# Optimization experiments

Measured on AMD Instinct MI355X. Metric: run time of the kernel, lower is better.

## Reference

```python
import jax, jax.numpy as jnp
import numpy as np

B_SZ, L_SEQ, D_MODEL, D_STATE = 4, 2048, 1024, 16


def setup_inputs() -> dict:
    key = jax.random.key(0)
    ks = jax.random.split(key, 6)
    x = jax.random.normal(ks[0], (B_SZ, L_SEQ, D_MODEL), jnp.float32)
    # HiPPO-inspired init: A_log = log(arange(1..n)).clamp(min=-7), broadcast over channels
    A_log = jnp.clip(jnp.log(jnp.arange(1, D_STATE + 1, dtype=jnp.float32)), -7.0, None)
    A_log = jnp.broadcast_to(A_log[None, :], (D_MODEL, D_STATE)).astype(jnp.float32)
    B_param = 0.02 * jax.random.normal(ks[1], (D_MODEL, D_STATE), jnp.float32)
    C_param = 0.02 * jax.random.normal(ks[2], (D_MODEL, D_STATE), jnp.float32)
    log_dt = 0.01 * jax.random.normal(ks[3], (D_MODEL,), jnp.float32) - 4.0
    in_w = jax.random.normal(ks[4], (2 * D_MODEL, D_MODEL), jnp.float32) / np.sqrt(D_MODEL).astype(np.float32)
    in_b = jnp.zeros((2 * D_MODEL,), jnp.float32)
    out_w = jax.random.normal(ks[5], (D_MODEL, D_MODEL), jnp.float32) / np.sqrt(D_MODEL).astype(np.float32)
    out_b = jnp.zeros((D_MODEL,), jnp.float32)
    ln_g = jnp.ones((D_MODEL,), jnp.float32)
    ln_b = jnp.zeros((D_MODEL,), jnp.float32)
    return {"x": x, "A_log": A_log, "B_param": B_param, "C_param": C_param,
            "log_dt": log_dt, "in_w": in_w, "in_b": in_b, "out_w": out_w,
            "out_b": out_b, "ln_g": ln_g, "ln_b": ln_b}


def _ssm_scan(u, A_log, B_param, C_param, log_dt):
    # u: (B, L, D). Builds kernel h[t,d] = sum_n A_bar[d,n]^t * C[d,n]*B[d,n]*dt[d]
    # and applies a causal depthwise convolution (via FFT; same math as conv1d).
    L = u.shape[1]
    dt = jnp.clip(jnp.exp(log_dt), 1e-4, 1.0)                      # (D,)
    A_bar = jnp.exp(-jnp.exp(A_log) * dt[:, None])                 # ZOH discretisation (D,N)
    A_bar = jnp.clip(A_bar, 1e-8, 1.0 - 1e-8)
    log_A = jnp.log(A_bar)                                         # (D,N)
    t_idx = jnp.arange(L, dtype=jnp.float32)                       # (L,)
    A_powers = jnp.exp(t_idx[:, None, None] * log_A[None, :, :])   # (L,D,N)
    cb_dt = C_param * B_param * dt[:, None]                        # (D,N)
    kernel = jnp.einsum('ldn,dn->ld', A_powers, cb_dt)             # (L,D)
    # causal conv: y[b,t,d] = sum_{tau<=t} kernel[tau,d] * u[b,t-tau,d]
    n_fft = 2 * L
    Kf = jnp.fft.rfft(kernel, n=n_fft, axis=0)                     # (n_fft/2+1, D)
    Uf = jnp.fft.rfft(u, n=n_fft, axis=1)                          # (B, n_fft/2+1, D)
    y = jnp.fft.irfft(Uf * Kf[None], n=n_fft, axis=1)[:, :L]       # (B,L,D)
    return y.astype(u.dtype)


def reference(x, A_log, B_param, C_param, log_dt, in_w, in_b, out_w, out_b, ln_g, ln_b):
    x = x.astype(jnp.float32)
    residual = x
    # LayerNorm (eps=1e-5)
    mu = jnp.mean(x, axis=-1, keepdims=True)
    var = jnp.mean(jnp.square(x - mu), axis=-1, keepdims=True)
    xn = (x - mu) * jax.lax.rsqrt(var + 1e-5) * ln_g + ln_b
    xz = xn @ in_w.T + in_b                                        # (B,L,2D)
    x_proj, z = xz[..., :D_MODEL], xz[..., D_MODEL:]
    z = jax.nn.silu(z)
    y = _ssm_scan(x_proj, A_log, B_param, C_param, log_dt)
    y = y * z
    y = y @ out_w.T + out_b
    # dropout is identity in eval mode
    return jnp.clip(y + residual, -10.0, 10.0)
```

## Files before the change

### kernel.cpp

```cpp
#include <hip/hip_runtime.h>
#include <hip/hip_bf16.h>

#define D_MODEL 1024
#define D_STATE 16
#define L_SEQ 2048
#define B_SZ 4
#define M_ROWS (B_SZ * L_SEQ)
#define N_CHUNK 32
#define C_LEN 64

typedef __attribute__((ext_vector_type(8))) short short8;
typedef __attribute__((ext_vector_type(4))) float f32x4;

#define SBAR()  asm volatile("s_barrier" ::: "memory")
#define GATE(N) asm volatile("s_waitcnt vmcnt(" #N ") lgkmcnt(0)\n\ts_barrier" ::: "memory")

typedef const unsigned short __attribute__((address_space(1))) gas_us;
typedef unsigned short __attribute__((address_space(3))) las_us;
static __device__ __forceinline__ void gload16(const unsigned short* g, unsigned short* l) {
    __builtin_amdgcn_global_load_lds((gas_us*)g, (las_us*)l, 16, 0, 0);
}

static __device__ __forceinline__ unsigned short f2bf(float f) {
    unsigned int u = __float_as_uint(f);
    unsigned int r = (u + 0x7FFFu + ((u >> 16) & 1u)) >> 16;
    return (unsigned short)r;
}
static __device__ __forceinline__ float bf2f(unsigned short u) {
    return __uint_as_float(((unsigned int)u) << 16);
}

__global__ __launch_bounds__(256) void prep_kernel(const float* __restrict__ x,
                                                   const float* __restrict__ g,
                                                   const float* __restrict__ b,
                                                   unsigned short* __restrict__ xn,
                                                   const float* __restrict__ in_w,
                                                   unsigned short* __restrict__ w1,
                                                   const float* __restrict__ out_w,
                                                   unsigned short* __restrict__ w2) {
    __shared__ float sbuf[8];
    int bid = blockIdx.x;
    int t = threadIdx.x;
    if (bid < M_ROWS) {
        int row = bid;
        const float4* xr = (const float4*)(x + (size_t)row * D_MODEL);
        float4 v = xr[t];
        float s  = v.x + v.y + v.z + v.w;
        float ss = v.x * v.x + v.y * v.y + v.z * v.z + v.w * v.w;
        #pragma unroll
        for (int o = 32; o > 0; o >>= 1) {
            s  += __shfl_down(s,  o);
            ss += __shfl_down(ss, o);
        }
        int wid = t >> 6;
        if ((t & 63) == 0) { sbuf[wid] = s; sbuf[4 + wid] = ss; }
        __syncthreads();
        float S  = sbuf[0] + sbuf[1] + sbuf[2] + sbuf[3];
        float SS = sbuf[4] + sbuf[5] + sbuf[6] + sbuf[7];
        float mu  = S * (1.0f / D_MODEL);
        float var = SS * (1.0f / D_MODEL) - mu * mu;
        float inv = rsqrtf(var + 1e-5f);
        float4 gv = ((const float4*)g)[t];
        float4 bv = ((const float4*)b)[t];
        ushort4 o;
        o.x = f2bf((v.x - mu) * inv * gv.x + bv.x);
        o.y = f2bf((v.y - mu) * inv * gv.y + bv.y);
        o.z = f2bf((v.z - mu) * inv * gv.z + bv.z);
        o.w = f2bf((v.w - mu) * inv * gv.w + bv.w);
        ((ushort4*)(xn + (size_t)row * D_MODEL))[t] = o;
    } else if (bid < M_ROWS + 2048) {
        int i = (bid - M_ROWS) * 256 + t;
        float4 v = ((const float4*)in_w)[i];
        ushort4 o;
        o.x = f2bf(v.x); o.y = f2bf(v.y); o.z = f2bf(v.z); o.w = f2bf(v.w);
        ((ushort4*)w1)[i] = o;
    } else {
        int i = (bid - M_ROWS - 2048) * 256 + t;
        float4 v = ((const float4*)out_w)[i];
        ushort4 o;
        o.x = f2bf(v.x); o.y = f2bf(v.y); o.z = f2bf(v.z); o.w = f2bf(v.w);
        ((ushort4*)w2)[i] = o;
    }
}

#define STG(B_, MAT_, KH_, GPTR_, KOFF_) do { \
    unsigned short* d_ = lbase + (B_)*32768 + (MAT_)*16384 + (KH_)*8192 + wave*1024; \
    gload16((GPTR_) + (KOFF_), d_); \
    gload16((GPTR_) + 16*K + (KOFF_), d_ + 512); } while(0)

#define PH(B_, KS_, MG_, READB_, STAGE_, TAIL_) { \
    if (READB_) { \
        _Pragma("unroll") for (int j_ = 0; j_ < 4; ++j_) \
            bv[j_] = *(const short8*)(ldsB + (B_)*65536 + (KS_)*16384 + (wn*4 + j_)*1024); \
    } \
    short8 av[4]; \
    _Pragma("unroll") for (int i_ = 0; i_ < 4; ++i_) \
        av[i_] = *(const short8*)(ldsA + (B_)*65536 + (KS_)*16384 + (wm*8 + (MG_)*4 + i_)*1024); \
    STAGE_; \
    SBAR(); \
    asm volatile("s_waitcnt lgkmcnt(0)" ::: "memory"); \
    __builtin_amdgcn_s_setprio(1); \
    _Pragma("unroll") for (int i_ = 0; i_ < 4; ++i_) { \
        _Pragma("unroll") for (int j_ = 0; j_ < 4; ++j_) \
            acc[(MG_)*4 + i_][j_] = __builtin_amdgcn_mfma_f32_16x16x32_bf16( \
                av[i_], bv[j_], acc[(MG_)*4 + i_][j_], 0, 0, 0); } \
    __builtin_amdgcn_s_setprio(0); \
    TAIL_; \
}

__global__ __launch_bounds__(512, 1) void gemm1_kernel(const unsigned short* __restrict__ A,
                                                       const unsigned short* __restrict__ Bt,
                                                       const float* __restrict__ bias,
                                                       unsigned short* __restrict__ u_bf,
                                                       unsigned short* __restrict__ zs) {
    __shared__ __align__(16) unsigned short lds[2][32768];
    const int K = D_MODEL;

    int t = threadIdx.x;
    int lane = t & 63;
    int wave = t >> 6;
    int wm = wave >> 2;
    int wn = wave & 3;

    int bid = blockIdx.x;
    int swz = (bid & 7) * 32 + (bid >> 3);
    int m0 = (swz >> 3) * 256;
    int n0 = (swz & 7) * 256;

    int srow = lane >> 2;
    int sk = ((lane & 3) * 8) ^ ((lane & 32) >> 1);
    const unsigned short* gA = A  + (size_t)(m0 + wave * 32 + srow) * K + sk;
    const unsigned short* gB = Bt + (size_t)(n0 + wave * 32 + srow) * K + sk;

    unsigned short* lbase = &lds[0][0];

    int off_base = (lane & 15) * 64 + (((lane >> 4) * 16) ^ ((lane & 8) * 4));
    const char* ldsA = (const char*)lbase + off_base;
    const char* ldsB = (const char*)lbase + 32768 + off_base;

    f32x4 acc[8][4] = {};
    short8 bv[4];

    STG(0, 0, 0, gA, 0);  STG(0, 1, 0, gB, 0);
    STG(0, 0, 1, gA, 32); STG(0, 1, 1, gB, 32);
    STG(1, 0, 0, gA, 64); STG(1, 1, 0, gB, 64);
    GATE(4);

    int ko = 0;
    #pragma unroll 1
    for (int it = 0; it < 7; ++it) {
        PH(0, 0, 0, true,  STG(1, 0, 1, gA, ko + 96),  SBAR());
        PH(0, 0, 1, false, STG(1, 1, 1, gB, ko + 96),  SBAR());
        PH(0, 1, 0, true,  STG(0, 0, 0, gA, ko + 128), SBAR());
        PH(0, 1, 1, false, STG(0, 1, 0, gB, ko + 128), GATE(4));
        PH(1, 0, 0, true,  STG(0, 0, 1, gA, ko + 160), SBAR());
        PH(1, 0, 1, false, STG(0, 1, 1, gB, ko + 160), SBAR());
        PH(1, 1, 0, true,  STG(1, 0, 0, gA, ko + 192), SBAR());
        PH(1, 1, 1, false, STG(1, 1, 0, gB, ko + 192), GATE(4));
        ko += 128;
    }
    PH(0, 0, 0, true,  STG(1, 0, 1, gA, ko + 96), SBAR());
    PH(0, 0, 1, false, STG(1, 1, 1, gB, ko + 96), SBAR());
    PH(0, 1, 0, true,  (void)0, SBAR());
    PH(0, 1, 1, false, (void)0, GATE(0));
    PH(1, 0, 0, true,  (void)0, SBAR());
    PH(1, 0, 1, false, (void)0, SBAR());
    PH(1, 1, 0, true,  (void)0, SBAR());
    PH(1, 1, 1, false, (void)0, (void)0);

    int col = lane & 15;
    int quad = lane >> 4;
    float bs[4];
    #pragma unroll
    for (int jf = 0; jf < 4; ++jf) bs[jf] = bias[n0 + wn * 64 + jf * 16 + col];
    bool isU = (n0 < D_MODEL);
    int nbase = isU ? (n0 + wn * 64 + col) : (n0 - D_MODEL + wn * 64 + col);
    unsigned short* obase = isU ? u_bf : zs;
    #pragma unroll
    for (int i = 0; i < 8; ++i) {
        #pragma unroll
        for (int r = 0; r < 4; ++r) {
            int m = m0 + wm * 128 + i * 16 + quad * 4 + r;
            unsigned short* orow = obase + (size_t)m * D_MODEL + nbase;
            #pragma unroll
            for (int jf = 0; jf < 4; ++jf) {
                float v = acc[i][jf][r] + bs[jf];
                if (!isU) v = v / (1.0f + __expf(-v));
                orow[jf * 16] = f2bf(v);
            }
        }
    }
}

#define MFMA16(ACC, AV, BV) { \
    _Pragma("unroll") for (int i_ = 0; i_ < 4; ++i_) { \
        _Pragma("unroll") for (int jf_ = 0; jf_ < 4; ++jf_) \
            ACC[i_][jf_] = __builtin_amdgcn_mfma_f32_16x16x32_bf16( \
                AV[i_], BV[jf_], ACC[i_][jf_], 0, 0, 0); } }

#define STAGE2(J) { size_t ko_ = (size_t)(J) * 32; int so_ = ((J) & 3) * 12288; \
    gload16(pA0 + ko_, dA + so_); gload16(pB0 + ko_, dB0 + so_); gload16(pB1 + ko_, dB1 + so_); }

#define G2_TILE(J, DOSTAGE, TRAIL) { \
    const int slot_ = (J) & 3; \
    const char* rA_ = ldsA_rd + slot_ * 24576; \
    const char* rB_ = ldsB_rd + slot_ * 24576; \
    short8 av[4], bv[4]; \
    _Pragma("unroll") for (int i_ = 0; i_ < 4; ++i_) av[i_] = *(const short8*)(rA_ + i_ * 1024); \
    _Pragma("unroll") for (int j_ = 0; j_ < 4; ++j_) bv[j_] = *(const short8*)(rB_ + j_ * 1024); \
    if (DOSTAGE) { STAGE2((J) + 3); } \
    SBAR(); \
    __builtin_amdgcn_s_setprio(1); \
    MFMA16(acc, av, bv); \
    __builtin_amdgcn_s_setprio(0); \
    TRAIL; \
}

__global__ __launch_bounds__(512, 2) void gemm2_kernel(const unsigned short* __restrict__ A,
                                                       const unsigned short* __restrict__ Bt,
                                                       const float* __restrict__ bias,
                                                       float* __restrict__ out_f,
                                                       const float* __restrict__ resid) {
    __shared__ __align__(16) unsigned short lds[4][12288];
    const int K = D_MODEL;

    int t = threadIdx.x;
    int lane = t & 63;
    int wave = t >> 6;
    int wm = wave >> 2;
    int wn = wave & 3;

    int bid = blockIdx.x;
    int swz = (bid & 7) * 32 + (bid >> 3);
    int m0 = (swz >> 2) * 128;
    int n0 = (swz & 3) * 256;

    int srow = lane >> 2;
    int sk = ((lane & 3) * 8) ^ ((lane & 32) >> 1);
    const unsigned short* pA0 = A  + (size_t)(m0 + wave * 16 + srow) * K + sk;
    const unsigned short* pB0 = Bt + (size_t)(n0 + wave * 16 + srow) * K + sk;
    const unsigned short* pB1 = pB0 + (size_t)128 * K;

    unsigned short* dA  = &lds[0][wave * 512];
    unsigned short* dB0 = &lds[0][4096 + wave * 512];
    unsigned short* dB1 = &lds[0][8192 + wave * 512];

    int off_base = (lane & 15) * 64 + (((lane >> 4) * 16) ^ ((lane & 8) * 4));
    const char* ldsA_rd = (const char*)(&lds[0][0]) + wm * 4096 + off_base;
    const char* ldsB_rd = (const char*)(&lds[0][0]) + 8192 + wn * 4096 + off_base;

    f32x4 acc[4][4] = {};

    STAGE2(0); STAGE2(1); STAGE2(2);
    GATE(6);

    #pragma unroll 1
    for (int j = 0; j < 29; ++j) { G2_TILE(j, true, GATE(6)); }
    G2_TILE(29, false, GATE(3));
    G2_TILE(30, false, GATE(0));
    G2_TILE(31, false, (void)0);

    int col = lane & 15;
    int quad = lane >> 4;
    float bs[4];
    #pragma unroll
    for (int jf = 0; jf < 4; ++jf) bs[jf] = bias[n0 + wn * 64 + jf * 16 + col];
    #pragma unroll
    for (int i = 0; i < 4; ++i) {
        #pragma unroll
        for (int r = 0; r < 4; ++r) {
            int m = m0 + wm * 64 + i * 16 + quad * 4 + r;
            const float* rrow = resid + (size_t)m * D_MODEL + n0 + wn * 64 + col;
            float* orow = out_f + (size_t)m * D_MODEL + n0 + wn * 64 + col;
            #pragma unroll
            for (int jf = 0; jf < 4; ++jf) {
                float y = acc[i][jf][r] + bs[jf] + rrow[jf * 16];
                y = fminf(10.0f, fmaxf(-10.0f, y));
                orow[jf * 16] = y;
            }
        }
    }
}

__global__ __launch_bounds__(512) void scan_fused_kernel(const unsigned short* __restrict__ u,
                                                         const unsigned short* __restrict__ zs,
                                                         const float* __restrict__ A_log,
                                                         const float* __restrict__ Bp,
                                                         const float* __restrict__ Cp,
                                                         const float* __restrict__ log_dt,
                                                         unsigned short* __restrict__ yz) {
    __shared__ __align__(16) unsigned short uslab[L_SEQ * 16];
    __shared__ float S[N_CHUNK][D_STATE][17];

    int bid = blockIdx.x;
    int l  = (bid & 7) * 32 + (bid >> 3);
    int b  = l >> 6;
    int dg = l & 63;
    int t  = threadIdx.x;
    int c  = t >> 4;
    int dl = t & 15;
    int d  = dg * 16 + dl;
    int lane = t & 63;
    int wave = t >> 6;

    {
        const unsigned short* src = u + ((size_t)b * L_SEQ + wave * 32 + (lane >> 1)) * D_MODEL
                                      + dg * 16 + (lane & 1) * 8;
        #pragma unroll
        for (int i = 0; i < 8; ++i)
            gload16(src + (size_t)i * 256 * D_MODEL, uslab + (i * 256 + wave * 32) * 16);
    }

    float dt = fminf(1.0f, fmaxf(1e-4f, __expf(log_dt[d])));
    float ab[D_STATE];
    #pragma unroll
    for (int n = 0; n < D_STATE; n++) {
        float a = __expf(-__expf(A_log[d * D_STATE + n]) * dt);
        ab[n] = fminf(1.0f - 1e-8f, fmaxf(1e-8f, a));
    }
    float cb[D_STATE];
    #pragma unroll
    for (int n = 0; n < D_STATE; n++)
        cb[n] = Cp[d * D_STATE + n] * Bp[d * D_STATE + n] * dt;

    asm volatile("s_waitcnt vmcnt(0)" ::: "memory");
    __syncthreads();

    const unsigned short* rcol = uslab + (c * 64) * 16 + dl;
    float P[D_STATE];
    #pragma unroll
    for (int n = 0; n < D_STATE; n++) P[n] = 0.0f;
    #pragma unroll 4
    for (int tt = 0; tt < C_LEN; tt++) {
        float uv = bf2f(rcol[tt * 16]);
        #pragma unroll
        for (int n = 0; n < D_STATE; n++) P[n] = fmaf(ab[n], P[n], uv);
    }

    #pragma unroll
    for (int n = 0; n < D_STATE; n++) S[c][n][dl] = P[n];

    float m[D_STATE];
    #pragma unroll
    for (int n = 0; n < D_STATE; n++) {
        float a2 = ab[n];
        #pragma unroll
        for (int q = 0; q < 6; q++) a2 = a2 * a2;
        m[n] = a2;
    }
    __syncthreads();

    #pragma unroll
    for (int k = 1; k < N_CHUNK; k <<= 1) {
        float tmp[D_STATE];
        #pragma unroll
        for (int n = 0; n < D_STATE; n++) tmp[n] = (c >= k) ? S[c - k][n][dl] : 0.0f;
        __syncthreads();
        #pragma unroll
        for (int n = 0; n < D_STATE; n++) {
            P[n] = fmaf(m[n], tmp[n], P[n]);
            S[c][n][dl] = P[n];
        }
        #pragma unroll
        for (int n = 0; n < D_STATE; n++) m[n] = m[n] * m[n];
        __syncthreads();
    }

    float s2[D_STATE];
    #pragma unroll
    for (int n = 0; n < D_STATE; n++) s2[n] = (c == 0) ? 0.0f : S[c - 1][n][dl];

    unsigned short* wcol = uslab + (c * 64) * 16 + dl;
    #pragma unroll 4
    for (int tt = 0; tt < C_LEN; tt++) {
        float uv = bf2f(wcol[tt * 16]);
        #pragma unroll
        for (int n = 0; n < D_STATE; n++) s2[n] = fmaf(ab[n], s2[n], uv);
        float y = 0.0f;
        #pragma unroll
        for (int n = 0; n < D_STATE; n++) y = fmaf(cb[n], s2[n], y);
        wcol[tt * 16] = f2bf(y);
    }
    __syncthreads();

    {
        size_t gbase = (size_t)b * L_SEQ * D_MODEL + (size_t)dg * 16;
        #pragma unroll
        for (int i = 0; i < 8; ++i) {
            int idx = i * 512 + t;
            int row = idx >> 1, half = idx & 1;
            size_t go = gbase + (size_t)row * D_MODEL + half * 8;
            short8 zv = *(const short8*)(zs + go);
            short8 yv = *(const short8*)(uslab + idx * 8);
            short8 o;
            #pragma unroll
            for (int e = 0; e < 8; ++e)
                o[e] = (short)f2bf(bf2f((unsigned short)yv[e]) * bf2f((unsigned short)zv[e]));
            *(short8*)(yz + go) = o;
        }
    }
}

extern "C" void kernel_launch(void* const* d_in, const int* in_sizes, int n_in,
                              void* d_out, int out_size, void* d_ws, size_t ws_size,
                              hipStream_t stream) {
    const float* x       = (const float*)d_in[0];
    const float* A_log   = (const float*)d_in[1];
    const float* B_param = (const float*)d_in[2];
    const float* C_param = (const float*)d_in[3];
    const float* log_dt  = (const float*)d_in[4];
    const float* in_w    = (const float*)d_in[5];
    const float* in_b    = (const float*)d_in[6];
    const float* out_w   = (const float*)d_in[7];
    const float* out_b   = (const float*)d_in[8];
    const float* ln_g    = (const float*)d_in[9];
    const float* ln_b    = (const float*)d_in[10];
    float* out = (float*)d_out;

    char* ws = (char*)d_ws;
    size_t off = 0;
    unsigned short* xn = (unsigned short*)(ws + off); off += (size_t)M_ROWS * D_MODEL * 2;
    unsigned short* w1 = (unsigned short*)(ws + off); off += (size_t)2 * D_MODEL * D_MODEL * 2;
    unsigned short* u  = (unsigned short*)(ws + off); off += (size_t)M_ROWS * D_MODEL * 2;
    unsigned short* zs = (unsigned short*)(ws + off); off += (size_t)M_ROWS * D_MODEL * 2;
    unsigned short* yz = (unsigned short*)(ws + off); off += (size_t)M_ROWS * D_MODEL * 2;
    unsigned short* w2 = (unsigned short*)(ws + off); off += (size_t)D_MODEL * D_MODEL * 2;

    prep_kernel<<<M_ROWS + 2048 + 1024, 256, 0, stream>>>(x, ln_g, ln_b, xn, in_w, w1, out_w, w2);

    gemm1_kernel<<<256, 512, 0, stream>>>(xn, w1, in_b, u, zs);

    scan_fused_kernel<<<256, 512, 0, stream>>>(u, zs, A_log, B_param, C_param, log_dt, yz);

    gemm2_kernel<<<256, 512, 0, stream>>>(yz, w2, out_b, out, x);
}
```

Baseline: 199.3 us.

## Fuse all four stages into one cooperative persistent kernel with grid syncs

Replaces the four separate launches (prep, gemm1, scan, gemm2) with one cooperative kernel of 256 blocks that runs each stage in turn, separated by grid-wide syncs. The prep stage is regridded so each block normalises 32 rows and converts a slice of the weights. The aim is to remove launch gaps and kernel-boundary drains between stages. In exchange, every block waits at each grid barrier, and all stages are tied to one launch configuration with 128KB of static LDS at occupancy 1, whereas gemm2 previously used occupancy 2.

```diff
diff --git a/kernel.cpp b/kernel.cpp
--- a/kernel.cpp
+++ b/kernel.cpp
@@ -1,5 +1,8 @@
 #include <hip/hip_runtime.h>
 #include <hip/hip_bf16.h>
+#include <hip/hip_cooperative_groups.h>
+
+namespace cg = cooperative_groups;
 
 #define D_MODEL 1024
 #define D_STATE 16
@@ -28,59 +31,6 @@
 }
 static __device__ __forceinline__ float bf2f(unsigned short u) {
     return __uint_as_float(((unsigned int)u) << 16);
-}
-
-__global__ __launch_bounds__(256) void prep_kernel(const float* __restrict__ x,
-                                                   const float* __restrict__ g,
-                                                   const float* __restrict__ b,
-                                                   unsigned short* __restrict__ xn,
-                                                   const float* __restrict__ in_w,
-                                                   unsigned short* __restrict__ w1,
-                                                   const float* __restrict__ out_w,
-                                                   unsigned short* __restrict__ w2) {
-    __shared__ float sbuf[8];
-    int bid = blockIdx.x;
-    int t = threadIdx.x;
-    if (bid < M_ROWS) {
-        int row = bid;
-        const float4* xr = (const float4*)(x + (size_t)row * D_MODEL);
-        float4 v = xr[t];
-        float s  = v.x + v.y + v.z + v.w;
-        float ss = v.x * v.x + v.y * v.y + v.z * v.z + v.w * v.w;
-        #pragma unroll
-        for (int o = 32; o > 0; o >>= 1) {
-            s  += __shfl_down(s,  o);
-            ss += __shfl_down(ss, o);
-        }
-        int wid = t >> 6;
-        if ((t & 63) == 0) { sbuf[wid] = s; sbuf[4 + wid] = ss; }
-        __syncthreads();
-        float S  = sbuf[0] + sbuf[1] + sbuf[2] + sbuf[3];
-        float SS = sbuf[4] + sbuf[5] + sbuf[6] + sbuf[7];
-        float mu  = S * (1.0f / D_MODEL);
-        float var = SS * (1.0f / D_MODEL) - mu * mu;
-        float inv = rsqrtf(var + 1e-5f);
-        float4 gv = ((const float4*)g)[t];
-        float4 bv = ((const float4*)b)[t];
-        ushort4 o;
-        o.x = f2bf((v.x - mu) * inv * gv.x + bv.x);
-        o.y = f2bf((v.y - mu) * inv * gv.y + bv.y);
-        o.z = f2bf((v.z - mu) * inv * gv.z + bv.z);
-        o.w = f2bf((v.w - mu) * inv * gv.w + bv.w);
-        ((ushort4*)(xn + (size_t)row * D_MODEL))[t] = o;
-    } else if (bid < M_ROWS + 2048) {
-        int i = (bid - M_ROWS) * 256 + t;
-        float4 v = ((const float4*)in_w)[i];
-        ushort4 o;
-        o.x = f2bf(v.x); o.y = f2bf(v.y); o.z = f2bf(v.z); o.w = f2bf(v.w);
-        ((ushort4*)w1)[i] = o;
-    } else {
-        int i = (bid - M_ROWS - 2048) * 256 + t;
-        float4 v = ((const float4*)out_w)[i];
-        ushort4 o;
-        o.x = f2bf(v.x); o.y = f2bf(v.y); o.z = f2bf(v.z); o.w = f2bf(v.w);
-        ((ushort4*)w2)[i] = o;
-    }
 }
 
 #define STG(B_, MAT_, KH_, GPTR_, KOFF_) do { \
@@ -108,90 +58,6 @@
     TAIL_; \
 }
 
-__global__ __launch_bounds__(512, 1) void gemm1_kernel(const unsigned short* __restrict__ A,
-                                                       const unsigned short* __restrict__ Bt,
-                                                       const float* __restrict__ bias,
-                                                       unsigned short* __restrict__ u_bf,
-                                                       unsigned short* __restrict__ zs) {
-    __shared__ __align__(16) unsigned short lds[2][32768];
-    const int K = D_MODEL;
-
-    int t = threadIdx.x;
-    int lane = t & 63;
-    int wave = t >> 6;
-    int wm = wave >> 2;
-    int wn = wave & 3;
-
-    int bid = blockIdx.x;
-    int swz = (bid & 7) * 32 + (bid >> 3);
-    int m0 = (swz >> 3) * 256;
-    int n0 = (swz & 7) * 256;
-
-    int srow = lane >> 2;
-    int sk = ((lane & 3) * 8) ^ ((lane & 32) >> 1);
-    const unsigned short* gA = A  + (size_t)(m0 + wave * 32 + srow) * K + sk;
-    const unsigned short* gB = Bt + (size_t)(n0 + wave * 32 + srow) * K + sk;
-
-    unsigned short* lbase = &lds[0][0];
-
-    int off_base = (lane & 15) * 64 + (((lane >> 4) * 16) ^ ((lane & 8) * 4));
-    const char* ldsA = (const char*)lbase + off_base;
-    const char* ldsB = (const char*)lbase + 32768 + off_base;
-
-    f32x4 acc[8][4] = {};
-    short8 bv[4];
-
-    STG(0, 0, 0, gA, 0);  STG(0, 1, 0, gB, 0);
-    STG(0, 0, 1, gA, 32); STG(0, 1, 1, gB, 32);
-    STG(1, 0, 0, gA, 64); STG(1, 1, 0, gB, 64);
-    GATE(4);
-
-    int ko = 0;
-    #pragma unroll 1
-    for (int it = 0; it < 7; ++it) {
-        PH(0, 0, 0, true,  STG(1, 0, 1, gA, ko + 96),  SBAR());
-        PH(0, 0, 1, false, STG(1, 1, 1, gB, ko + 96),  SBAR());
-        PH(0, 1, 0, true,  STG(0, 0, 0, gA, ko + 128), SBAR());
-        PH(0, 1, 1, false, STG(0, 1, 0, gB, ko + 128), GATE(4));
-        PH(1, 0, 0, true,  STG(0, 0, 1, gA, ko + 160), SBAR());
-        PH(1, 0, 1, false, STG(0, 1, 1, gB, ko + 160), SBAR());
-        PH(1, 1, 0, true,  STG(1, 0, 0, gA, ko + 192), SBAR());
-        PH(1, 1, 1, false, STG(1, 1, 0, gB, ko + 192), GATE(4));
-        ko += 128;
-    }
-    PH(0, 0, 0, true,  STG(1, 0, 1, gA, ko + 96), SBAR());
-    PH(0, 0, 1, false, STG(1, 1, 1, gB, ko + 96), SBAR());
-    PH(0, 1, 0, true,  (void)0, SBAR());
-    PH(0, 1, 1, false, (void)0, GATE(0));
-    PH(1, 0, 0, true,  (void)0, SBAR());
-    PH(1, 0, 1, false, (void)0, SBAR());
-    PH(1, 1, 0, true,  (void)0, SBAR());
-    PH(1, 1, 1, false, (void)0, (void)0);
-
-    int col = lane & 15;
-    int quad = lane >> 4;
-    float bs[4];
-    #pragma unroll
-    for (int jf = 0; jf < 4; ++jf) bs[jf] = bias[n0 + wn * 64 + jf * 16 + col];
-    bool isU = (n0 < D_MODEL);
-    int nbase = isU ? (n0 + wn * 64 + col) : (n0 - D_MODEL + wn * 64 + col);
-    unsigned short* obase = isU ? u_bf : zs;
-    #pragma unroll
-    for (int i = 0; i < 8; ++i) {
-        #pragma unroll
-        for (int r = 0; r < 4; ++r) {
-            int m = m0 + wm * 128 + i * 16 + quad * 4 + r;
-            unsigned short* orow = obase + (size_t)m * D_MODEL + nbase;
-            #pragma unroll
-            for (int jf = 0; jf < 4; ++jf) {
-                float v = acc[i][jf][r] + bs[jf];
-                if (!isU) v = v / (1.0f + __expf(-v));
-                orow[jf * 16] = f2bf(v);
-            }
-        }
-    }
-}
-
 #define MFMA16(ACC, AV, BV) { \
     _Pragma("unroll") for (int i_ = 0; i_ < 4; ++i_) { \
         _Pragma("unroll") for (int jf_ = 0; jf_ < 4; ++jf_) \
@@ -216,187 +82,321 @@
     TRAIL; \
 }
 
-__global__ __launch_bounds__(512, 2) void gemm2_kernel(const unsigned short* __restrict__ A,
-                                                       const unsigned short* __restrict__ Bt,
-                                                       const float* __restrict__ bias,
-                                                       float* __restrict__ out_f,
-                                                       const float* __restrict__ resid) {
-    __shared__ __align__(16) unsigned short lds[4][12288];
-    const int K = D_MODEL;
-
+__global__ __launch_bounds__(512, 1) void mega_kernel(
+    const float* __restrict__ x, const float* __restrict__ A_log,
+    const float* __restrict__ Bp, const float* __restrict__ Cp,
+    const float* __restrict__ log_dt, const float* __restrict__ in_w,
+    const float* __restrict__ in_b, const float* __restrict__ out_w,
+    const float* __restrict__ out_b, const float* __restrict__ ln_g,
+    const float* __restrict__ ln_b, float* __restrict__ out,
+    unsigned short* __restrict__ xn, unsigned short* __restrict__ w1,
+    unsigned short* __restrict__ u, unsigned short* __restrict__ zs,
+    unsigned short* __restrict__ yz, unsigned short* __restrict__ w2)
+{
+    __shared__ __align__(16) unsigned char smem[131072];
+    cg::grid_group grid = cg::this_grid();
+
+    int bid = blockIdx.x;
     int t = threadIdx.x;
     int lane = t & 63;
     int wave = t >> 6;
-    int wm = wave >> 2;
-    int wn = wave & 3;
-
-    int bid = blockIdx.x;
-    int swz = (bid & 7) * 32 + (bid >> 3);
-    int m0 = (swz >> 2) * 128;
-    int n0 = (swz & 3) * 256;
-
-    int srow = lane >> 2;
-    int sk = ((lane & 3) * 8) ^ ((lane & 32) >> 1);
-    const unsigned short* pA0 = A  + (size_t)(m0 + wave * 16 + srow) * K + sk;
-    const unsigned short* pB0 = Bt + (size_t)(n0 + wave * 16 + srow) * K + sk;
-    const unsigned short* pB1 = pB0 + (size_t)128 * K;
-
-    unsigned short* dA  = &lds[0][wave * 512];
-    unsigned short* dB0 = &lds[0][4096 + wave * 512];
-    unsigned short* dB1 = &lds[0][8192 + wave * 512];
-
-    int off_base = (lane & 15) * 64 + (((lane >> 4) * 16) ^ ((lane & 8) * 4));
-    const char* ldsA_rd = (const char*)(&lds[0][0]) + wm * 4096 + off_base;
-    const char* ldsB_rd = (const char*)(&lds[0][0]) + 8192 + wn * 4096 + off_base;
-
-    f32x4 acc[4][4] = {};
-
-    STAGE2(0); STAGE2(1); STAGE2(2);
-    GATE(6);
-
-    #pragma unroll 1
-    for (int j = 0; j < 29; ++j) { G2_TILE(j, true, GATE(6)); }
-    G2_TILE(29, false, GATE(3));
-    G2_TILE(30, false, GATE(0));
-    G2_TILE(31, false, (void)0);
-
-    int col = lane & 15;
-    int quad = lane >> 4;
-    float bs[4];
-    #pragma unroll
-    for (int jf = 0; jf < 4; ++jf) bs[jf] = bias[n0 + wn * 64 + jf * 16 + col];
-    #pragma unroll
-    for (int i = 0; i < 4; ++i) {
-        #pragma unroll
-        for (int r = 0; r < 4; ++r) {
-            int m = m0 + wm * 64 + i * 16 + quad * 4 + r;
-            const float* rrow = resid + (size_t)m * D_MODEL + n0 + wn * 64 + col;
-            float* orow = out_f + (size_t)m * D_MODEL + n0 + wn * 64 + col;
-            #pragma unroll
-            for (int jf = 0; jf < 4; ++jf) {
-                float y = acc[i][jf][r] + bs[jf] + rrow[jf * 16];
-                y = fminf(10.0f, fmaxf(-10.0f, y));
-                orow[jf * 16] = y;
+
+    {
+        float* sred = (float*)smem;
+        int sb = t >> 8;
+        int tt = t & 255;
+        #pragma unroll 1
+        for (int i = 0; i < 16; ++i) {
+            int row = bid * 32 + i * 2 + sb;
+            const float4* xr = (const float4*)(x + (size_t)row * D_MODEL);
+            float4 v = xr[tt];
+            float s  = v.x + v.y + v.z + v.w;
+            float ss = v.x * v.x + v.y * v.y + v.z * v.z + v.w * v.w;
+            #pragma unroll
+            for (int o = 32; o > 0; o >>= 1) {
+                s  += __shfl_down(s,  o);
+                ss += __shfl_down(ss, o);
+            }
+            int wid = tt >> 6;
+            if ((tt & 63) == 0) { sred[sb * 8 + wid] = s; sred[sb * 8 + 4 + wid] = ss; }
+            __syncthreads();
+            float S  = sred[sb * 8 + 0] + sred[sb * 8 + 1] + sred[sb * 8 + 2] + sred[sb * 8 + 3];
+            float SS = sred[sb * 8 + 4] + sred[sb * 8 + 5] + sred[sb * 8 + 6] + sred[sb * 8 + 7];
+            float mu  = S * (1.0f / D_MODEL);
+            float var = SS * (1.0f / D_MODEL) - mu * mu;
+            float inv = rsqrtf(var + 1e-5f);
+            float4 gv = ((const float4*)ln_g)[tt];
+            float4 bv = ((const float4*)ln_b)[tt];
+            ushort4 o;
+            o.x = f2bf((v.x - mu) * inv * gv.x + bv.x);
+            o.y = f2bf((v.y - mu) * inv * gv.y + bv.y);
+            o.z = f2bf((v.z - mu) * inv * gv.z + bv.z);
+            o.w = f2bf((v.w - mu) * inv * gv.w + bv.w);
+            ((ushort4*)(xn + (size_t)row * D_MODEL))[tt] = o;
+            __syncthreads();
+        }
+        int idx = bid * 512 + t;
+        #pragma unroll
+        for (int k2 = 0; k2 < 6; ++k2) {
+            int j = k2 * 131072 + idx;
+            if (j < 524288) {
+                float4 v = ((const float4*)in_w)[j];
+                ushort4 o;
+                o.x = f2bf(v.x); o.y = f2bf(v.y); o.z = f2bf(v.z); o.w = f2bf(v.w);
+                ((ushort4*)w1)[j] = o;
+            } else {
+                int j2 = j - 524288;
+                float4 v = ((const float4*)out_w)[j2];
+                ushort4 o;
+                o.x = f2bf(v.x); o.y = f2bf(v.y); o.z = f2bf(v.z); o.w = f2bf(v.w);
+                ((ushort4*)w2)[j2] = o;
             }
         }
     }
-}
-
-__global__ __launch_bounds__(512) void scan_fused_kernel(const unsigned short* __restrict__ u,
-                                                         const unsigned short* __restrict__ zs,
-                                                         const float* __restrict__ A_log,
-                                                         const float* __restrict__ Bp,
-                                                         const float* __restrict__ Cp,
-                                                         const float* __restrict__ log_dt,
-                                                         unsigned short* __restrict__ yz) {
-    __shared__ __align__(16) unsigned short uslab[L_SEQ * 16];
-    __shared__ float S[N_CHUNK][D_STATE][17];
-
-    int bid = blockIdx.x;
-    int l  = (bid & 7) * 32 + (bid >> 3);
-    int b  = l >> 6;
-    int dg = l & 63;
-    int t  = threadIdx.x;
-    int c  = t >> 4;
-    int dl = t & 15;
-    int d  = dg * 16 + dl;
-    int lane = t & 63;
-    int wave = t >> 6;
+    __threadfence();
+    grid.sync();
+    __threadfence();
 
     {
-        const unsigned short* src = u + ((size_t)b * L_SEQ + wave * 32 + (lane >> 1)) * D_MODEL
-                                      + dg * 16 + (lane & 1) * 8;
-        #pragma unroll
-        for (int i = 0; i < 8; ++i)
-            gload16(src + (size_t)i * 256 * D_MODEL, uslab + (i * 256 + wave * 32) * 16);
+        const int K = D_MODEL;
+        int wm = wave >> 2;
+        int wn = wave & 3;
+        int swz = (bid & 7) * 32 + (bid >> 3);
+        int m0 = (swz >> 3) * 256;
+        int n0 = (swz & 7) * 256;
+
+        int srow = lane >> 2;
+        int sk = ((lane & 3) * 8) ^ ((lane & 32) >> 1);
+        const unsigned short* gA = xn + (size_t)(m0 + wave * 32 + srow) * K + sk;
+        const unsigned short* gB = w1 + (size_t)(n0 + wave * 32 + srow) * K + sk;
+
+        unsigned short* lbase = (unsigned short*)smem;
+        int off_base = (lane & 15) * 64 + (((lane >> 4) * 16) ^ ((lane & 8) * 4));
+        const char* ldsA = (const char*)lbase + off_base;
+        const char* ldsB = (const char*)lbase + 32768 + off_base;
+
+        f32x4 acc[8][4] = {};
+        short8 bv[4];
+
+        STG(0, 0, 0, gA, 0);  STG(0, 1, 0, gB, 0);
+        STG(0, 0, 1, gA, 32); STG(0, 1, 1, gB, 32);
+        STG(1, 0, 0, gA, 64); STG(1, 1, 0, gB, 64);
+        GATE(4);
+
+        int ko = 0;
+        #pragma unroll 1
+        for (int it = 0; it < 7; ++it) {
+            PH(0, 0, 0, true,  STG(1, 0, 1, gA, ko + 96),  SBAR());
+            PH(0, 0, 1, false, STG(1, 1, 1, gB, ko + 96),  SBAR());
+            PH(0, 1, 0, true,  STG(0, 0, 0, gA, ko + 128), SBAR());
+            PH(0, 1, 1, false, STG(0, 1, 0, gB, ko + 128), GATE(4));
+            PH(1, 0, 0, true,  STG(0, 0, 1, gA, ko + 160), SBAR());
+            PH(1, 0, 1, false, STG(0, 1, 1, gB, ko + 160), SBAR());
+            PH(1, 1, 0, true,  STG(1, 0, 0, gA, ko + 192), SBAR());
+            PH(1, 1, 1, false, STG(1, 1, 0, gB, ko + 192), GATE(4));
+            ko += 128;
+        }
+        PH(0, 0, 0, true,  STG(1, 0, 1, gA, ko + 96), SBAR());
+        PH(0, 0, 1, false, STG(1, 1, 1, gB, ko + 96), SBAR());
+        PH(0, 1, 0, true,  (void)0, SBAR());
+        PH(0, 1, 1, false, (void)0, GATE(0));
+        PH(1, 0, 0, true,  (void)0, SBAR());
+        PH(1, 0, 1, false, (void)0, SBAR());
+        PH(1, 1, 0, true,  (void)0, SBAR());
+        PH(1, 1, 1, false, (void)0, (void)0);
+
+        int col = lane & 15;
+        int quad = lane >> 4;
+        float bs[4];
+        #pragma unroll
+        for (int jf = 0; jf < 4; ++jf) bs[jf] = in_b[n0 + wn * 64 + jf * 16 + col];
+        bool isU = (n0 < D_MODEL);
+        int nbase = isU ? (n0 + wn * 64 + col) : (n0 - D_MODEL + wn * 64 + col);
+        unsigned short* obase = isU ? u : zs;
+        #pragma unroll
+        for (int i = 0; i < 8; ++i) {
+            #pragma unroll
+            for (int r = 0; r < 4; ++r) {
+                int m = m0 + wm * 128 + i * 16 + quad * 4 + r;
+                unsigned short* orow = obase + (size_t)m * D_MODEL + nbase;
+                #pragma unroll
+                for (int jf = 0; jf < 4; ++jf) {
+                    float v = acc[i][jf][r] + bs[jf];
+                    if (!isU) v = v / (1.0f + __expf(-v));
+                    orow[jf * 16] = f2bf(v);
+                }
+            }
+        }
     }
-
-    float dt = fminf(1.0f, fmaxf(1e-4f, __expf(log_dt[d])));
-    float ab[D_STATE];
-    #pragma unroll
-    for (int n = 0; n < D_STATE; n++) {
-        float a = __expf(-__expf(A_log[d * D_STATE + n]) * dt);
-        ab[n] = fminf(1.0f - 1e-8f, fmaxf(1e-8f, a));
+    __threadfence();
+    grid.sync();
+    __threadfence();
+
+    {
+        unsigned short* uslab = (unsigned short*)smem;
+        float (*S)[D_STATE][17] = reinterpret_cast<float (*)[D_STATE][17]>(smem + 65536);
+
+        int l  = (bid & 7) * 32 + (bid >> 3);
+        int b  = l >> 6;
+        int dg = l & 63;
+        int c  = t >> 4;
+        int dl = t & 15;
+        int d  = dg * 16 + dl;
+
+        {
+            const unsigned short* src = u + ((size_t)b * L_SEQ + wave * 32 + (lane >> 1)) * D_MODEL
+                                          + dg * 16 + (lane & 1) * 8;
+            #pragma unroll
+            for (int i = 0; i < 8; ++i)
+                gload16(src + (size_t)i * 256 * D_MODEL, uslab + (i * 256 + wave * 32) * 16);
+        }
+
+        float dt = fminf(1.0f, fmaxf(1e-4f, __expf(log_dt[d])));
+        float ab[D_STATE];
+        #pragma unroll
+        for (int n = 0; n < D_STATE; n++) {
+            float a = __expf(-__expf(A_log[d * D_STATE + n]) * dt);
+            ab[n] = fminf(1.0f - 1e-8f, fmaxf(1e-8f, a));
+        }
+        float cb[D_STATE];
+        #pragma unroll
+        for (int n = 0; n < D_STATE; n++)
+            cb[n] = Cp[d * D_STATE + n] * Bp[d * D_STATE + n] * dt;
+
+        asm volatile("s_waitcnt vmcnt(0)" ::: "memory");
+        __syncthreads();
+
+        const unsigned short* rcol = uslab + (c * 64) * 16 + dl;
+        float P[D_STATE];
+        #pragma unroll
+        for (int n = 0; n < D_STATE; n++) P[n] = 0.0f;
+        #pragma unroll 4
+        for (int tt = 0; tt < C_LEN; tt++) {
+            float uv = bf2f(rcol[tt * 16]);
+            #pragma unroll
+            for (int n = 0; n < D_STATE; n++) P[n] = fmaf(ab[n], P[n], uv);
+        }
+
+        #pragma unroll
+        for (int n = 0; n < D_STATE; n++) S[c][n][dl] = P[n];
+
+        float m[D_STATE];
+        #pragma unroll
+        for (int n = 0; n < D_STATE; n++) {
+            float a2 = ab[n];
+            #pragma unroll
+            for (int q = 0; q < 6; q++) a2 = a2 * a2;
+            m[n] = a2;
+        }
+        __syncthreads();
+
+        #pragma unroll
+        for (int k = 1; k < N_CHUNK; k <<= 1) {
+            float tmp[D_STATE];
+            #pragma unroll
+            for (int n = 0; n < D_STATE; n++) tmp[n] = (c >= k) ? S[c - k][n][dl] : 0.0f;
+            __syncthreads();
+            #pragma unroll
+            for (int n = 0; n < D_STATE; n++) {
+                P[n] = fmaf(m[n], tmp[n], P[n]);
+                S[c][n][dl] = P[n];
+            }
+            #pragma unroll
+            for (int n = 0; n < D_STATE; n++) m[n] = m[n] * m[n];
+            __syncthreads();
+        }
+
+        float s2[D_STATE];
+        #pragma unroll
+        for (int n = 0; n < D_STATE; n++) s2[n] = (c == 0) ? 0.0f : S[c - 1][n][dl];
+
+        unsigned short* wcol = uslab + (c * 64) * 16 + dl;
+        #pragma unroll 4
+        for (int tt = 0; tt < C_LEN; tt++) {
+            float uv = bf2f(wcol[tt * 16]);
+            #pragma unroll
+            for (int n = 0; n < D_STATE; n++) s2[n] = fmaf(ab[n], s2[n], uv);
+            float y = 0.0f;
+            #pragma unroll
+            for (int n = 0; n < D_STATE; n++) y = fmaf(cb[n], s2[n], y);
+            wcol[tt * 16] = f2bf(y);
+        }
+        __syncthreads();
+
+        {
+            size_t gbase = (size_t)b * L_SEQ * D_MODEL + (size_t)dg * 16;
+            #pragma unroll
+            for (int i = 0; i < 8; ++i) {
+                int idx = i * 512 + t;
+                int row = idx >> 1, half = idx & 1;
+                size_t go = gbase + (size_t)row * D_MODEL + half * 8;
+                short8 zv = *(const short8*)(zs + go);
+                short8 yv = *(const short8*)(uslab + idx * 8);
+                short8 o;
+                #pragma unroll
+                for (int e = 0; e < 8; ++e)
+                    o[e] = (short)f2bf(bf2f((unsigned short)yv[e]) * bf2f((unsigned short)zv[e]));
+                *(short8*)(yz + go) = o;
+            }
+        }
     }
-    float cb[D_STATE];
-    #pragma unroll
-    for (int n = 0; n < D_STATE; n++)
-        cb[n] = Cp[d * D_STATE + n] * Bp[d * D_STATE + n] * dt;
-
-    asm volatile("s_waitcnt vmcnt(0)" ::: "memory");
-    __syncthreads();
-
-    const unsigned short* rcol = uslab + (c * 64) * 16 + dl;
-    float P[D_STATE];
-    #pragma unroll
-    for (int n = 0; n < D_STATE; n++) P[n] = 0.0f;
-    #pragma unroll 4
-    for (int tt = 0; tt < C_LEN; tt++) {
-        float uv = bf2f(rcol[tt * 16]);
-        #pragma unroll
-        for (int n = 0; n < D_STATE; n++) P[n] = fmaf(ab[n], P[n], uv);
-    }
-
-    #pragma unroll
-    for (int n = 0; n < D_STATE; n++) S[c][n][dl] = P[n];
-
-    float m[D_STATE];
-    #pragma unroll
-    for (int n = 0; n < D_STATE; n++) {
-        float a2 = ab[n];
-        #pragma unroll
-        for (int q = 0; q < 6; q++) a2 = a2 * a2;
-        m[n] = a2;
-    }
-    __syncthreads();
-
-    #pragma unroll
-    for (int k = 1; k < N_CHUNK; k <<= 1) {
-        float tmp[D_STATE];
-        #pragma unroll
-        for (int n = 0; n < D_STATE; n++) tmp[n] = (c >= k) ? S[c - k][n][dl] : 0.0f;
-        __syncthreads();
-        #pragma unroll
-        for (int n = 0; n < D_STATE; n++) {
-            P[n] = fmaf(m[n], tmp[n], P[n]);
-            S[c][n][dl] = P[n];
-        }
-        #pragma unroll
-        for (int n = 0; n < D_STATE; n++) m[n] = m[n] * m[n];
-        __syncthreads();
-    }
-
-    float s2[D_STATE];
-    #pragma unroll
-    for (int n = 0; n < D_STATE; n++) s2[n] = (c == 0) ? 0.0f : S[c - 1][n][dl];
-
-    unsigned short* wcol = uslab + (c * 64) * 16 + dl;
-    #pragma unroll 4
-    for (int tt = 0; tt < C_LEN; tt++) {
-        float uv = bf2f(wcol[tt * 16]);
-        #pragma unroll
-        for (int n = 0; n < D_STATE; n++) s2[n] = fmaf(ab[n], s2[n], uv);
-        float y = 0.0f;
-        #pragma unroll
-        for (int n = 0; n < D_STATE; n++) y = fmaf(cb[n], s2[n], y);
-        wcol[tt * 16] = f2bf(y);
-    }
-    __syncthreads();
+    __threadfence();
+    grid.sync();
+    __threadfence();
 
     {
-        size_t gbase = (size_t)b * L_SEQ * D_MODEL + (size_t)dg * 16;
-        #pragma unroll
-        for (int i = 0; i < 8; ++i) {
-            int idx = i * 512 + t;
-            int row = idx >> 1, half = idx & 1;
-            size_t go = gbase + (size_t)row * D_MODEL + half * 8;
-            short8 zv = *(const short8*)(zs + go);
-            short8 yv = *(const short8*)(uslab + idx * 8);
-            short8 o;
-            #pragma unroll
-            for (int e = 0; e < 8; ++e)
-                o[e] = (short)f2bf(bf2f((unsigned short)yv[e]) * bf2f((unsigned short)zv[e]));
-            *(short8*)(yz + go) = o;
+        const int K = D_MODEL;
+        int wm = wave >> 2;
+        int wn = wave & 3;
+        int swz = (bid & 7) * 32 + (bid >> 3);
+        int m0 = (swz >> 2) * 128;
+        int n0 = (swz & 3) * 256;
+
+        int srow = lane >> 2;
+        int sk = ((lane & 3) * 8) ^ ((lane & 32) >> 1);
+        const unsigned short* pA0 = yz + (size_t)(m0 + wave * 16 + srow) * K + sk;
+        const unsigned short* pB0 = w2 + (size_t)(n0 + wave * 16 + srow) * K + sk;
+        const unsigned short* pB1 = pB0 + (size_t)128 * K;
+
+        unsigned short* lds2 = (unsigned short*)smem;
+        unsigned short* dA  = lds2 + wave * 512;
+        unsigned short* dB0 = lds2 + 4096 + wave * 512;
+        unsigned short* dB1 = lds2 + 8192 + wave * 512;
+
+        int off_base = (lane & 15) * 64 + (((lane >> 4) * 16) ^ ((lane & 8) * 4));
+        const char* ldsA_rd = (const char*)lds2 + wm * 4096 + off_base;
+        const char* ldsB_rd = (const char*)lds2 + 8192 + wn * 4096 + off_base;
+
+        f32x4 acc[4][4] = {};
+
+        STAGE2(0); STAGE2(1); STAGE2(2);
+        GATE(6);
+
+        #pragma unroll 1
+        for (int j = 0; j < 29; ++j) { G2_TILE(j, true, GATE(6)); }
+        G2_TILE(29, false, GATE(3));
+        G2_TILE(30, false, GATE(0));
+        G2_TILE(31, false, (void)0);
+
+        int col = lane & 15;
+        int quad = lane >> 4;
+        float bs[4];
+        #pragma unroll
+        for (int jf = 0; jf < 4; ++jf) bs[jf] = out_b[n0 + wn * 64 + jf * 16 + col];
+        #pragma unroll
+        for (int i = 0; i < 4; ++i) {
+            #pragma unroll
+            for (int r = 0; r < 4; ++r) {
+                int m = m0 + wm * 64 + i * 16 + quad * 4 + r;
+                const float* rrow = x + (size_t)m * D_MODEL + n0 + wn * 64 + col;
+                float* orow = out + (size_t)m * D_MODEL + n0 + wn * 64 + col;
+                #pragma unroll
+                for (int jf = 0; jf < 4; ++jf) {
+                    float y = acc[i][jf][r] + bs[jf] + rrow[jf * 16];
+                    y = fminf(10.0f, fmaxf(-10.0f, y));
+                    orow[jf * 16] = y;
+                }
+            }
         }
     }
 }
@@ -426,11 +426,12 @@
     unsigned short* yz = (unsigned short*)(ws + off); off += (size_t)M_ROWS * D_MODEL * 2;
     unsigned short* w2 = (unsigned short*)(ws + off); off += (size_t)D_MODEL * D_MODEL * 2;
 
-    prep_kernel<<<M_ROWS + 2048 + 1024, 256, 0, stream>>>(x, ln_g, ln_b, xn, in_w, w1, out_w, w2);
-
-    gemm1_kernel<<<256, 512, 0, stream>>>(xn, w1, in_b, u, zs);
-
-    scan_fused_kernel<<<256, 512, 0, stream>>>(u, zs, A_log, B_param, C_param, log_dt, yz);
-
-    gemm2_kernel<<<256, 512, 0, stream>>>(yz, w2, out_b, out, x);
-}
+    void* kargs[] = {
+        (void*)&x, (void*)&A_log, (void*)&B_param, (void*)&C_param, (void*)&log_dt,
+        (void*)&in_w, (void*)&in_b, (void*)&out_w, (void*)&out_b, (void*)&ln_g,
+        (void*)&ln_b, (void*)&out, (void*)&xn, (void*)&w1, (void*)&u, (void*)&zs,
+        (void*)&yz, (void*)&w2
+    };
+    hipLaunchCooperativeKernel(reinterpret_cast<void*>(mega_kernel),
+                               dim3(256), dim3(512), kargs, 0, stream);
+}
```

Result: slower. 608.7 us (+205.5%).
